# Optimization experiments

Hardware: AMD Instinct MI355X
Metric: run time of the kernel (lower is better)

## Reference

```python
import jax, jax.numpy as jnp
import numpy as np

B, T, C, H = 32, 2048, 1024, 64


def setup_inputs() -> dict:
    key = jax.random.key(0)
    k1, k2, k3, k4 = jax.random.split(key, 4)
    x = jax.random.normal(k1, (B, T, C), dtype=jnp.float32)
    # nn.Linear(C, H, bias=False) weights, stored here as [C, H] for x @ W
    s = 1.0 / np.sqrt(C)
    Wk = jax.random.uniform(k2, (C, H), jnp.float32, -s, s)
    Wq = jax.random.uniform(k3, (C, H), jnp.float32, -s, s)
    Wv = jax.random.uniform(k4, (C, H), jnp.float32, -s, s)
    return {"x": x, "Wk": Wk, "Wq": Wq, "Wv": Wv}


def reference(x, Wk, Wq, Wv):
    # projections: [B,T,C] @ [C,H] -> [B,T,H]
    k = jnp.einsum('btc,ch->bth', x, Wk)
    q = jnp.einsum('btc,ch->bth', x, Wq)
    v = jnp.einsum('btc,ch->bth', x, Wv)
    Hd = k.shape[-1]
    # attention scores [B,T,T], scaled by head_size^-0.5
    scores = jnp.einsum('bqh,bkh->bqk', q, k) * (Hd ** -0.5)
    # causal mask: masked_fill where triu(ones, 1)==1 -> -inf (mask strict upper triangle)
    Tq = x.shape[1]
    causal = jnp.tril(jnp.ones((Tq, Tq), dtype=bool))  # True = keep
    scores = jnp.where(causal, scores, -jnp.inf)
    attn = jax.nn.softmax(scores, axis=-1)
    # dropout: identity in eval/reference mode
    out = jnp.einsum('bqk,bkh->bqh', attn, v)
    return out
```

## Files before the change

### kernel.cpp

```cpp
#include <hip/hip_runtime.h>
#include <hip/hip_bf16.h>

typedef short bf16x8 __attribute__((ext_vector_type(8)));
typedef float f32x4 __attribute__((ext_vector_type(4)));

#define B_ 32
#define T_ 2048
#define C_ 1024
#define H_ 64

__device__ __forceinline__ ushort f2bf(float f) {
  union { float f; unsigned u; } v; v.f = f;
  unsigned u = v.u;
  return (ushort)((u + 0x7FFFu + ((u >> 16) & 1u)) >> 16);
}

__device__ __forceinline__ bf16x8 pack8(float4 a, float4 b) {
  union { __hip_bfloat162 h; short2 s; } t;
  bf16x8 r;
  t.h = __float22bfloat162_rn(make_float2(a.x, a.y)); r[0] = t.s.x; r[1] = t.s.y;
  t.h = __float22bfloat162_rn(make_float2(a.z, a.w)); r[2] = t.s.x; r[3] = t.s.y;
  t.h = __float22bfloat162_rn(make_float2(b.x, b.y)); r[4] = t.s.x; r[5] = t.s.y;
  t.h = __float22bfloat162_rn(make_float2(b.z, b.w)); r[6] = t.s.x; r[7] = t.s.y;
  return r;
}

__device__ __forceinline__ void async_copy16(void* lds, const void* g) {
  __builtin_amdgcn_global_load_lds(
      (const __attribute__((address_space(1))) unsigned int*)g,
      (__attribute__((address_space(3))) unsigned int*)lds, 16, 0, 0);
}

__global__ __launch_bounds__(256) void wconv_kernel(
    const float* __restrict__ Wk, const float* __restrict__ Wq,
    const float* __restrict__ Wv, ushort* __restrict__ Wt) {
  int idx = blockIdx.x * 256 + threadIdx.x;
  if (idx >= 3 * 64 * C_) return;
  int n = idx >> 10, c = idx & 1023;
  int mat = n >> 6, h = n & 63;
  const float* W = (mat == 0) ? Wk : (mat == 1 ? Wq : Wv);
  float v = W[c * 64 + h];
  if (mat == 1) v *= 0.18033688011112042f;
  Wt[idx] = f2bf(v);
}

__global__ __launch_bounds__(256, 4) void qkv_kernel(
    const float* __restrict__ x, const ushort* __restrict__ Wt,
    ushort* __restrict__ Kb, ushort* __restrict__ Qb, ushort* __restrict__ Vt) {
  __shared__ __align__(16) ushort Bs[192 * 64];
  int tid = threadIdx.x;
  int wave = tid >> 6, lane = tid & 63, quad = lane >> 4, l16 = lane & 15;
  int r0 = blockIdx.x * 64;
  const float* xr = x + (size_t)(r0 + wave * 16 + l16) * C_;

  f32x4 acc[12];
#pragma unroll
  for (int nt = 0; nt < 12; ++nt) acc[nt] = (f32x4){0.f, 0.f, 0.f, 0.f};

  for (int k0 = 0; k0 < C_; k0 += 64) {
    __syncthreads();
#pragma unroll
    for (int i = 0; i < 6; ++i) {
      int id = tid + 256 * i;
      int n = id >> 3, p = id & 7, c = p ^ (n & 7);
      async_copy16((char*)Bs + id * 16, Wt + (size_t)n * C_ + k0 + c * 8);
    }
    float4 a0 = *(const float4*)(xr + k0 + quad * 8);
    float4 a1 = *(const float4*)(xr + k0 + quad * 8 + 4);
    float4 a2 = *(const float4*)(xr + k0 + 32 + quad * 8);
    float4 a3 = *(const float4*)(xr + k0 + 32 + quad * 8 + 4);
    __syncthreads();

    bf16x8 af0 = pack8(a0, a1);
    bf16x8 af1 = pack8(a2, a3);
#pragma unroll
    for (int nt = 0; nt < 12; ++nt) {
      int n = nt * 16 + l16;
      bf16x8 b0 = *(const bf16x8*)(Bs + n * 64 + ((quad ^ (l16 & 7)) << 3));
      bf16x8 b1 = *(const bf16x8*)(Bs + n * 64 + (((4 + quad) ^ (l16 & 7)) << 3));
      acc[nt] = __builtin_amdgcn_mfma_f32_16x16x32_bf16(af0, b0, acc[nt], 0, 0, 0);
      acc[nt] = __builtin_amdgcn_mfma_f32_16x16x32_bf16(af1, b1, acc[nt], 0, 0, 0);
    }
  }

  int b = r0 >> 11;
  int rowbase = r0 + wave * 16 + quad * 4;
#pragma unroll
  for (int nt = 0; nt < 12; ++nt) {
    int mat = nt >> 2;
    int h = (nt & 3) * 16 + l16;
    if (mat == 2) {
      ushort4 pv;
      pv.x = f2bf(acc[nt][0]); pv.y = f2bf(acc[nt][1]);
      pv.z = f2bf(acc[nt][2]); pv.w = f2bf(acc[nt][3]);
      *(ushort4*)(&Vt[(size_t)b * H_ * T_ + (size_t)h * T_ + (rowbase & (T_ - 1))]) = pv;
    } else {
      ushort* dst = (mat == 0) ? Kb : Qb;
#pragma unroll
      for (int r = 0; r < 4; ++r)
        dst[(size_t)(rowbase + r) * H_ + h] = f2bf(acc[nt][r]);
    }
  }
}

__global__ __launch_bounds__(256, 4) void attn_kernel(
    const ushort* __restrict__ Qb, const ushort* __restrict__ Kb,
    const ushort* __restrict__ Vt, float* __restrict__ out) {
  __shared__ __align__(16) ushort Ks[64 * 64];
  __shared__ __align__(16) ushort Vs[64 * 64];
  __shared__ __align__(16) ushort Pl[4 * 16 * 80];

  int tid = threadIdx.x;
  int wave = tid >> 6, lane = tid & 63, quad = lane >> 4, l16 = lane & 15;
  int bx = blockIdx.x, by = blockIdx.y;
  int batch = (bx & 7) + 8 * (by & 3);
  int qseg = 31 - ((bx >> 3) + 4 * (by >> 2));
  int q0 = qseg * 64 + wave * 16;
  const ushort* Qbase = Qb + (size_t)batch * T_ * H_;
  const ushort* Kbase = Kb + (size_t)batch * T_ * H_;
  const ushort* Vbase = Vt + (size_t)batch * H_ * T_;
  ushort* Pw = Pl + wave * 16 * 80;

  const ushort* qr = Qbase + (size_t)(q0 + l16) * H_;
  bf16x8 qf0 = *(const bf16x8*)(qr + quad * 8);
  bf16x8 qf1 = *(const bf16x8*)(qr + 32 + quad * 8);

  f32x4 o[4];
  float m_i[4], l_i[4];
#pragma unroll
  for (int i = 0; i < 4; ++i) {
    o[i] = (f32x4){0.f, 0.f, 0.f, 0.f};
    m_i[i] = -1e30f; l_i[i] = 0.f;
  }

  int jb_last = qseg;
  for (int jb = 0; jb <= jb_last; ++jb) {
    int j0 = jb * 64;
    __syncthreads();
#pragma unroll
    for (int g = 0; g < 2; ++g) {
      int id = tid + 256 * g;
      int r = id >> 3, p = id & 7, c = p ^ (r & 7);
      async_copy16((char*)Ks + id * 16, Kbase + (size_t)(j0 + r) * H_ + c * 8);
      async_copy16((char*)Vs + id * 16, Vbase + (size_t)r * T_ + j0 + c * 8);
    }
    __syncthreads();

    f32x4 sv[4];
#pragma unroll
    for (int nt = 0; nt < 4; ++nt) {
      int n = nt * 16 + l16;
      bf16x8 kf0 = *(const bf16x8*)(Ks + n * 64 + ((quad ^ (l16 & 7)) << 3));
      bf16x8 kf1 = *(const bf16x8*)(Ks + n * 64 + (((4 + quad) ^ (l16 & 7)) << 3));
      f32x4 z = (f32x4){0.f, 0.f, 0.f, 0.f};
      z = __builtin_amdgcn_mfma_f32_16x16x32_bf16(qf0, kf0, z, 0, 0, 0);
      z = __builtin_amdgcn_mfma_f32_16x16x32_bf16(qf1, kf1, z, 0, 0, 0);
      sv[nt] = z;
    }

    if (jb == jb_last) {
      int rowg = q0 + quad * 4;
#pragma unroll
      for (int nt = 0; nt < 4; ++nt) {
        int col = j0 + nt * 16 + l16;
#pragma unroll
        for (int rr = 0; rr < 4; ++rr)
          if (col > rowg + rr) sv[nt][rr] = -1e30f;
      }
    }

    float alpha[4];
#pragma unroll
    for (int rr = 0; rr < 4; ++rr) {
      float v = fmaxf(fmaxf(sv[0][rr], sv[1][rr]), fmaxf(sv[2][rr], sv[3][rr]));
      v = fmaxf(v, __shfl_xor(v, 1));
      v = fmaxf(v, __shfl_xor(v, 2));
      v = fmaxf(v, __shfl_xor(v, 4));
      v = fmaxf(v, __shfl_xor(v, 8));
      float mn = fmaxf(m_i[rr], v);
      alpha[rr] = exp2f(m_i[rr] - mn);
      m_i[rr] = mn;
    }
    float rsum[4] = {0.f, 0.f, 0.f, 0.f};
#pragma unroll
    for (int nt = 0; nt < 4; ++nt)
#pragma unroll
      for (int rr = 0; rr < 4; ++rr) {
        float p = exp2f(sv[nt][rr] - m_i[rr]);
        rsum[rr] += p;
        Pw[(quad * 4 + rr) * 80 + nt * 16 + l16] = f2bf(p);
      }
#pragma unroll
    for (int rr = 0; rr < 4; ++rr) l_i[rr] = alpha[rr] * l_i[rr] + rsum[rr];
#pragma unroll
    for (int ht = 0; ht < 4; ++ht)
#pragma unroll
      for (int rr = 0; rr < 4; ++rr) o[ht][rr] *= alpha[rr];

    bf16x8 pf0 = *(const bf16x8*)(&Pw[l16 * 80 + quad * 8]);
    bf16x8 pf1 = *(const bf16x8*)(&Pw[l16 * 80 + 32 + quad * 8]);
#pragma unroll
    for (int ht = 0; ht < 4; ++ht) {
      int hrow = ht * 16 + l16;
      bf16x8 vf0 = *(const bf16x8*)(Vs + hrow * 64 + ((quad ^ (l16 & 7)) << 3));
      bf16x8 vf1 = *(const bf16x8*)(Vs + hrow * 64 + (((4 + quad) ^ (l16 & 7)) << 3));
      o[ht] = __builtin_amdgcn_mfma_f32_16x16x32_bf16(pf0, vf0, o[ht], 0, 0, 0);
      o[ht] = __builtin_amdgcn_mfma_f32_16x16x32_bf16(pf1, vf1, o[ht], 0, 0, 0);
    }
  }

#pragma unroll
  for (int rr = 0; rr < 4; ++rr) {
    float v = l_i[rr];
    v += __shfl_xor(v, 1);
    v += __shfl_xor(v, 2);
    v += __shfl_xor(v, 4);
    v += __shfl_xor(v, 8);
    l_i[rr] = __builtin_amdgcn_rcpf(v);
  }
  int rowbase = q0 + quad * 4;
#pragma unroll
  for (int ht = 0; ht < 4; ++ht)
#pragma unroll
    for (int rr = 0; rr < 4; ++rr)
      out[((size_t)batch * T_ + rowbase + rr) * H_ + ht * 16 + l16] =
          o[ht][rr] * l_i[rr];
}

extern "C" void kernel_launch(void* const* d_in, const int* in_sizes, int n_in,
                              void* d_out, int out_size, void* d_ws, size_t ws_size,
                              hipStream_t stream) {
  const float* x  = (const float*)d_in[0];
  const float* Wk = (const float*)d_in[1];
  const float* Wq = (const float*)d_in[2];
  const float* Wv = (const float*)d_in[3];
  float* out = (float*)d_out;

  ushort* Wt = (ushort*)d_ws;
  ushort* Kb = (ushort*)((char*)d_ws + (1 << 19));
  ushort* Qb = Kb + (size_t)B_ * T_ * H_;
  ushort* Vt = Qb + (size_t)B_ * T_ * H_;

  hipLaunchKernelGGL(wconv_kernel, dim3(768), dim3(256), 0, stream, Wk, Wq, Wv, Wt);
  hipLaunchKernelGGL(qkv_kernel, dim3(1024), dim3(256), 0, stream, x, Wt, Kb, Qb, Vt);
  hipLaunchKernelGGL(attn_kernel, dim3(32, 32), dim3(256), 0, stream, Qb, Kb, Vt, out);
}
```

Before: 451.4 us.

## Pair causal q-segments per block, double-buffer K/V tiles, lazy softmax rescale

```diff
diff --git a/kernel.cpp b/kernel.cpp
--- a/kernel.cpp
+++ b/kernel.cpp
@@ -103,128 +103,152 @@
   }
 }
 
-__global__ __launch_bounds__(256, 4) void attn_kernel(
+__global__ __launch_bounds__(256, 2) void attn_kernel(
     const ushort* __restrict__ Qb, const ushort* __restrict__ Kb,
     const ushort* __restrict__ Vt, float* __restrict__ out) {
-  __shared__ __align__(16) ushort Ks[64 * 64];
-  __shared__ __align__(16) ushort Vs[64 * 64];
+  __shared__ __align__(16) ushort Ks[2][64 * 64];
+  __shared__ __align__(16) ushort Vs[2][64 * 64];
   __shared__ __align__(16) ushort Pl[4 * 16 * 80];
 
   int tid = threadIdx.x;
   int wave = tid >> 6, lane = tid & 63, quad = lane >> 4, l16 = lane & 15;
-  int bx = blockIdx.x, by = blockIdx.y;
-  int batch = (bx & 7) + 8 * (by & 3);
-  int qseg = 31 - ((bx >> 3) + 4 * (by >> 2));
-  int q0 = qseg * 64 + wave * 16;
+  int bid = blockIdx.x;
+  int xcd = bid & 7, wi = bid >> 3;
+  int batch = xcd * 4 + (wi & 3);
+  int spair = wi >> 2;
   const ushort* Qbase = Qb + (size_t)batch * T_ * H_;
   const ushort* Kbase = Kb + (size_t)batch * T_ * H_;
   const ushort* Vbase = Vt + (size_t)batch * H_ * T_;
   ushort* Pw = Pl + wave * 16 * 80;
 
-  const ushort* qr = Qbase + (size_t)(q0 + l16) * H_;
-  bf16x8 qf0 = *(const bf16x8*)(qr + quad * 8);
-  bf16x8 qf1 = *(const bf16x8*)(qr + 32 + quad * 8);
-
-  f32x4 o[4];
-  float m_i[4], l_i[4];
-#pragma unroll
-  for (int i = 0; i < 4; ++i) {
-    o[i] = (f32x4){0.f, 0.f, 0.f, 0.f};
-    m_i[i] = -1e30f; l_i[i] = 0.f;
-  }
-
-  int jb_last = qseg;
-  for (int jb = 0; jb <= jb_last; ++jb) {
+  auto stage = [&](int jb, int buf) {
     int j0 = jb * 64;
-    __syncthreads();
 #pragma unroll
     for (int g = 0; g < 2; ++g) {
       int id = tid + 256 * g;
       int r = id >> 3, p = id & 7, c = p ^ (r & 7);
-      async_copy16((char*)Ks + id * 16, Kbase + (size_t)(j0 + r) * H_ + c * 8);
-      async_copy16((char*)Vs + id * 16, Vbase + (size_t)r * T_ + j0 + c * 8);
-    }
+      async_copy16((char*)&Ks[buf][0] + id * 16,
+                   Kbase + (size_t)(j0 + r) * H_ + c * 8);
+      async_copy16((char*)&Vs[buf][0] + id * 16,
+                   Vbase + (size_t)r * T_ + j0 + c * 8);
+    }
+  };
+
+#pragma unroll 1
+  for (int half = 0; half < 2; ++half) {
+    int qseg = half ? spair : 31 - spair;
+    int q0 = qseg * 64 + wave * 16;
+    const ushort* qr = Qbase + (size_t)(q0 + l16) * H_;
+    bf16x8 qf0 = *(const bf16x8*)(qr + quad * 8);
+    bf16x8 qf1 = *(const bf16x8*)(qr + 32 + quad * 8);
+
+    f32x4 o[4];
+    float m_i[4], l_i[4];
+#pragma unroll
+    for (int i = 0; i < 4; ++i) {
+      o[i] = (f32x4){0.f, 0.f, 0.f, 0.f};
+      m_i[i] = -1e30f; l_i[i] = 0.f;
+    }
+
+    int jb_last = qseg;
     __syncthreads();
-
-    f32x4 sv[4];
-#pragma unroll
-    for (int nt = 0; nt < 4; ++nt) {
-      int n = nt * 16 + l16;
-      bf16x8 kf0 = *(const bf16x8*)(Ks + n * 64 + ((quad ^ (l16 & 7)) << 3));
-      bf16x8 kf1 = *(const bf16x8*)(Ks + n * 64 + (((4 + quad) ^ (l16 & 7)) << 3));
-      f32x4 z = (f32x4){0.f, 0.f, 0.f, 0.f};
-      z = __builtin_amdgcn_mfma_f32_16x16x32_bf16(qf0, kf0, z, 0, 0, 0);
-      z = __builtin_amdgcn_mfma_f32_16x16x32_bf16(qf1, kf1, z, 0, 0, 0);
-      sv[nt] = z;
-    }
-
-    if (jb == jb_last) {
-      int rowg = q0 + quad * 4;
+    stage(0, 0);
+    int cur = 0;
+    for (int jb = 0; jb <= jb_last; ++jb, cur ^= 1) {
+      int j0 = jb * 64;
+      __syncthreads();
+      if (jb < jb_last) stage(jb + 1, cur ^ 1);
+      const ushort* KsC = &Ks[cur][0];
+      const ushort* VsC = &Vs[cur][0];
+
+      f32x4 sv[4];
 #pragma unroll
       for (int nt = 0; nt < 4; ++nt) {
-        int col = j0 + nt * 16 + l16;
-#pragma unroll
-        for (int rr = 0; rr < 4; ++rr)
-          if (col > rowg + rr) sv[nt][rr] = -1e30f;
-      }
-    }
-
-    float alpha[4];
+        int n = nt * 16 + l16;
+        bf16x8 kf0 = *(const bf16x8*)(KsC + n * 64 + ((quad ^ (l16 & 7)) << 3));
+        bf16x8 kf1 = *(const bf16x8*)(KsC + n * 64 + (((4 + quad) ^ (l16 & 7)) << 3));
+        f32x4 z = (f32x4){0.f, 0.f, 0.f, 0.f};
+        z = __builtin_amdgcn_mfma_f32_16x16x32_bf16(qf0, kf0, z, 0, 0, 0);
+        z = __builtin_amdgcn_mfma_f32_16x16x32_bf16(qf1, kf1, z, 0, 0, 0);
+        sv[nt] = z;
+      }
+
+      if (jb == jb_last) {
+        int rowg = q0 + quad * 4;
+#pragma unroll
+        for (int nt = 0; nt < 4; ++nt) {
+          int col = j0 + nt * 16 + l16;
+#pragma unroll
+          for (int rr = 0; rr < 4; ++rr)
+            if (col > rowg + rr) sv[nt][rr] = -1e30f;
+        }
+      }
+
+      float pm[4];
+#pragma unroll
+      for (int rr = 0; rr < 4; ++rr) {
+        float v = fmaxf(fmaxf(sv[0][rr], sv[1][rr]), fmaxf(sv[2][rr], sv[3][rr]));
+        v = fmaxf(v, __shfl_xor(v, 1));
+        v = fmaxf(v, __shfl_xor(v, 2));
+        v = fmaxf(v, __shfl_xor(v, 4));
+        v = fmaxf(v, __shfl_xor(v, 8));
+        pm[rr] = v;
+      }
+      bool grow = (pm[0] > m_i[0] + 8.f) || (pm[1] > m_i[1] + 8.f) ||
+                  (pm[2] > m_i[2] + 8.f) || (pm[3] > m_i[3] + 8.f);
+      if (__any(grow)) {
+#pragma unroll
+        for (int rr = 0; rr < 4; ++rr) {
+          float mn = fmaxf(m_i[rr], pm[rr]);
+          float alpha = exp2f(m_i[rr] - mn);
+          m_i[rr] = mn;
+          l_i[rr] *= alpha;
+#pragma unroll
+          for (int ht = 0; ht < 4; ++ht) o[ht][rr] *= alpha;
+        }
+      }
+
+      float rsum[4] = {0.f, 0.f, 0.f, 0.f};
+#pragma unroll
+      for (int nt = 0; nt < 4; ++nt)
+#pragma unroll
+        for (int rr = 0; rr < 4; ++rr) {
+          float p = exp2f(sv[nt][rr] - m_i[rr]);
+          rsum[rr] += p;
+          Pw[(quad * 4 + rr) * 80 + nt * 16 + l16] = f2bf(p);
+        }
+#pragma unroll
+      for (int rr = 0; rr < 4; ++rr) l_i[rr] += rsum[rr];
+
+      bf16x8 pf0 = *(const bf16x8*)(&Pw[l16 * 80 + quad * 8]);
+      bf16x8 pf1 = *(const bf16x8*)(&Pw[l16 * 80 + 32 + quad * 8]);
+#pragma unroll
+      for (int ht = 0; ht < 4; ++ht) {
+        int hrow = ht * 16 + l16;
+        bf16x8 vf0 = *(const bf16x8*)(VsC + hrow * 64 + ((quad ^ (l16 & 7)) << 3));
+        bf16x8 vf1 = *(const bf16x8*)(VsC + hrow * 64 + (((4 + quad) ^ (l16 & 7)) << 3));
+        o[ht] = __builtin_amdgcn_mfma_f32_16x16x32_bf16(pf0, vf0, o[ht], 0, 0, 0);
+        o[ht] = __builtin_amdgcn_mfma_f32_16x16x32_bf16(pf1, vf1, o[ht], 0, 0, 0);
+      }
+    }
+
 #pragma unroll
     for (int rr = 0; rr < 4; ++rr) {
-      float v = fmaxf(fmaxf(sv[0][rr], sv[1][rr]), fmaxf(sv[2][rr], sv[3][rr]));
-      v = fmaxf(v, __shfl_xor(v, 1));
-      v = fmaxf(v, __shfl_xor(v, 2));
-      v = fmaxf(v, __shfl_xor(v, 4));
-      v = fmaxf(v, __shfl_xor(v, 8));
-      float mn = fmaxf(m_i[rr], v);
-      alpha[rr] = exp2f(m_i[rr] - mn);
-      m_i[rr] = mn;
-    }
-    float rsum[4] = {0.f, 0.f, 0.f, 0.f};
-#pragma unroll
-    for (int nt = 0; nt < 4; ++nt)
-#pragma unroll
-      for (int rr = 0; rr < 4; ++rr) {
-        float p = exp2f(sv[nt][rr] - m_i[rr]);
-        rsum[rr] += p;
-        Pw[(quad * 4 + rr) * 80 + nt * 16 + l16] = f2bf(p);
-      }
-#pragma unroll
-    for (int rr = 0; rr < 4; ++rr) l_i[rr] = alpha[rr] * l_i[rr] + rsum[rr];
+      float v = l_i[rr];
+      v += __shfl_xor(v, 1);
+      v += __shfl_xor(v, 2);
+      v += __shfl_xor(v, 4);
+      v += __shfl_xor(v, 8);
+      l_i[rr] = __builtin_amdgcn_rcpf(v);
+    }
+    int rowbase = q0 + quad * 4;
 #pragma unroll
     for (int ht = 0; ht < 4; ++ht)
 #pragma unroll
-      for (int rr = 0; rr < 4; ++rr) o[ht][rr] *= alpha[rr];
-
-    bf16x8 pf0 = *(const bf16x8*)(&Pw[l16 * 80 + quad * 8]);
-    bf16x8 pf1 = *(const bf16x8*)(&Pw[l16 * 80 + 32 + quad * 8]);
-#pragma unroll
-    for (int ht = 0; ht < 4; ++ht) {
-      int hrow = ht * 16 + l16;
-      bf16x8 vf0 = *(const bf16x8*)(Vs + hrow * 64 + ((quad ^ (l16 & 7)) << 3));
-      bf16x8 vf1 = *(const bf16x8*)(Vs + hrow * 64 + (((4 + quad) ^ (l16 & 7)) << 3));
-      o[ht] = __builtin_amdgcn_mfma_f32_16x16x32_bf16(pf0, vf0, o[ht], 0, 0, 0);
-      o[ht] = __builtin_amdgcn_mfma_f32_16x16x32_bf16(pf1, vf1, o[ht], 0, 0, 0);
-    }
+      for (int rr = 0; rr < 4; ++rr)
+        out[((size_t)batch * T_ + rowbase + rr) * H_ + ht * 16 + l16] =
+            o[ht][rr] * l_i[rr];
   }
-
-#pragma unroll
-  for (int rr = 0; rr < 4; ++rr) {
-    float v = l_i[rr];
-    v += __shfl_xor(v, 1);
-    v += __shfl_xor(v, 2);
-    v += __shfl_xor(v, 4);
-    v += __shfl_xor(v, 8);
-    l_i[rr] = __builtin_amdgcn_rcpf(v);
-  }
-  int rowbase = q0 + quad * 4;
-#pragma unroll
-  for (int ht = 0; ht < 4; ++ht)
-#pragma unroll
-    for (int rr = 0; rr < 4; ++rr)
-      out[((size_t)batch * T_ + rowbase + rr) * H_ + ht * 16 + l16] =
-          o[ht][rr] * l_i[rr];
 }
 
 extern "C" void kernel_launch(void* const* d_in, const int* in_sizes, int n_in,
@@ -243,5 +267,5 @@
 
   hipLaunchKernelGGL(wconv_kernel, dim3(768), dim3(256), 0, stream, Wk, Wq, Wv, Wt);
   hipLaunchKernelGGL(qkv_kernel, dim3(1024), dim3(256), 0, stream, x, Wt, Kb, Qb, Vt);
-  hipLaunchKernelGGL(attn_kernel, dim3(32, 32), dim3(256), 0, stream, Qb, Kb, Vt, out);
-}
+  hipLaunchKernelGGL(attn_kernel, dim3(512), dim3(256), 0, stream, Qb, Kb, Vt, out);
+}
```

New measurement: 442.1 us. -2.1%, faster.
